# Kernel tuning notes

Measured on AMD Instinct MI355X. Metric: run time of the kernel, lower is better.

## Reference

```python
import jax, jax.numpy as jnp
import numpy as np

# Analytic closed form of the 4-qubit circuit. Wires (0,1) and (2,3) are
# independent 2-qubit blocks: RY(x_a)oRY(x_b) -> CNOT(a,b) -> RY(p_a)oRY(p_b).
# Heisenberg picture gives:
#   <Z_a> = cos(p_a)*cos(x_a) + sin(p_a)*sin(x_a)*sin(x_b)
#   <Z_b> = cos(p_b)*cos(x_a)*cos(x_b) + sin(p_b)*sin(x_b)

def setup_inputs() -> dict:
    key = jax.random.key(0)
    k1, k2, k3, k4 = jax.random.split(key, 4)
    B = 16384
    return {
        "x": jax.random.uniform(k1, (B, 1, 28, 28), dtype=jnp.float32),
        "vqc_params": jax.random.normal(k2, (4,), dtype=jnp.float32),
        "fc_w": jax.random.normal(k3, (10, 784), dtype=jnp.float32) * 0.05,
        "fc_b": jax.random.normal(k4, (10,), dtype=jnp.float32) * 0.05,
        "bias": jnp.zeros((10,), dtype=jnp.float32),
    }


def _pair_expvals(xa, xb, pa, pb):
    # xa, xb: [B, 196]; pa, pb: scalars
    za = jnp.cos(pa) * jnp.cos(xa) + jnp.sin(pa) * jnp.sin(xa) * jnp.sin(xb)
    zb = jnp.cos(pb) * jnp.cos(xa) * jnp.cos(xb) + jnp.sin(pb) * jnp.sin(xb)
    return za, zb


def reference(x, vqc_params, fc_w, fc_b, bias):
    B = x.shape[0]
    # Extract 2x2 patches in the same (r, c) row-major order as the torch loop.
    # [B,28,28] -> [B,14,2,14,2] -> [B,14,14,2,2] -> [B,196,4]
    p = x[:, 0].reshape(B, 14, 2, 14, 2).transpose(0, 1, 3, 2, 4).reshape(B, 196, 4)
    x0, x1, x2, x3 = p[..., 0], p[..., 1], p[..., 2], p[..., 3]
    p0, p1, p2, p3 = vqc_params[0], vqc_params[1], vqc_params[2], vqc_params[3]
    z0, z1 = _pair_expvals(x0, x1, p0, p1)
    z2, z3 = _pair_expvals(x2, x3, p2, p3)
    q = jnp.stack([z0, z1, z2, z3], axis=-1).reshape(B, 4 * 196)  # patch-major, wire-minor
    logits = q @ fc_w.T + fc_b - bias
    return jax.nn.log_softmax(logits, axis=-1)
```

## Files before the change

kernel.cpp:

```cpp
#include <hip/hip_runtime.h>


typedef __attribute__((ext_vector_type(8))) short short8;
typedef __attribute__((ext_vector_type(4))) float f32x4;

constexpr int WAVES = 4;
constexpr int BLOCK = WAVES * 64;
constexpr int IMGS  = 16;
constexpr int NITER = 7;
constexpr int PF    = 4;

static __device__ __forceinline__ short f2bf(float f) {
    union { float f; unsigned u; } v; v.f = f;
    unsigned r = v.u + 0x7fffu + ((v.u >> 16) & 1u);
    return (short)(r >> 16);
}

__global__ __launch_bounds__(BLOCK, 4)
void quanv_mfma(const float* __restrict__ x,
                const float* __restrict__ vqc,
                const float* __restrict__ fc_w,
                const float* __restrict__ fc_b,
                const float* __restrict__ bias,
                float* __restrict__ out,
                int B)
{
    __shared__ float cpart[3][64 * 4];

    const int tid  = threadIdx.x;
    const int lane = tid & 63;
    const int wv   = tid >> 6;
    const int i16  = lane & 15;
    const int g    = lane >> 4;

    const int imgBase = blockIdx.x * IMGS;
    const int imgLane = imgBase + i16;
    const long xb = (long)(imgLane < B ? imgLane : B - 1) * 784;
    const float* __restrict__ xpb = x + xb;

    auto xoff = [&](int I) -> int {
        const int kb = wv + 4 * I;
        int j0 = kb * 8 + 2 * g;
        if (j0 > 194) j0 = 0;
        const int r = j0 / 14, c = j0 - 14 * r;
        return 56 * r + 2 * c;
    };

    float4 bT[PF], bB[PF];
    #pragma unroll
    for (int I = 0; I < PF; ++I) {
        const int o = xoff(I);
        bT[I] = *reinterpret_cast<const float4*>(xpb + o);
        bB[I] = *reinterpret_cast<const float4*>(xpb + o + 28);
    }

    float S0, C0, S1, C1, S2, C2, S3, C3;
    __sincosf(vqc[0], &S0, &C0);
    __sincosf(vqc[1], &S1, &C1);
    __sincosf(vqc[2], &S2, &C2);
    __sincosf(vqc[3], &S3, &C3);

    const int ncl = (i16 < 10) ? i16 : 9;
    const float* __restrict__ wrow = fc_w + ncl * 784;
    short8 bf[NITER];
    #pragma unroll
    for (int I = 0; I < NITER; ++I) {
        const int kb = wv + 4 * I;
        int k = kb * 32 + g * 8;
        if (k > 776) k = 776;
        const float4 lo = *reinterpret_cast<const float4*>(wrow + k);
        const float4 hi = *reinterpret_cast<const float4*>(wrow + k + 4);
        short8 t;
        t[0] = f2bf(lo.x); t[1] = f2bf(lo.y); t[2] = f2bf(lo.z); t[3] = f2bf(lo.w);
        t[4] = f2bf(hi.x); t[5] = f2bf(hi.y); t[6] = f2bf(hi.z); t[7] = f2bf(hi.w);
        bf[I] = t;
    }

    f32x4 acc = {0.f, 0.f, 0.f, 0.f};

    #pragma unroll
    for (int I = 0; I < NITER; ++I) {
        const float4 a4 = bT[I & 3];
        const float4 b4 = bB[I & 3];

        if (I + PF < NITER) {
            const int o = xoff(I + PF);
            bT[I & 3] = *reinterpret_cast<const float4*>(xpb + o);
            bB[I & 3] = *reinterpret_cast<const float4*>(xpb + o + 28);
        }

        const int   j0  = (wv + 4 * I) * 8 + 2 * g;
        const float msk = (j0 <= 194) ? 1.f : 0.f;

        float sa, ca, sb, cb, sc, cc, sd, cd;
        __sincosf(a4.x, &sa, &ca);  __sincosf(a4.y, &sb, &cb);
        __sincosf(b4.x, &sc, &cc);  __sincosf(b4.y, &sd, &cd);
        const float q0 = (C0 * ca + S0 * (sa * sb)) * msk;
        const float q1 = (C1 * (ca * cb) + S1 * sb) * msk;
        const float q2 = (C2 * cc + S2 * (sc * sd)) * msk;
        const float q3 = (C3 * (cc * cd) + S3 * sd) * msk;
        __sincosf(a4.z, &sa, &ca);  __sincosf(a4.w, &sb, &cb);
        __sincosf(b4.z, &sc, &cc);  __sincosf(b4.w, &sd, &cd);
        const float q4 = (C0 * ca + S0 * (sa * sb)) * msk;
        const float q5 = (C1 * (ca * cb) + S1 * sb) * msk;
        const float q6 = (C2 * cc + S2 * (sc * sd)) * msk;
        const float q7 = (C3 * (cc * cd) + S3 * sd) * msk;

        short8 a;
        a[0] = f2bf(q0); a[1] = f2bf(q1); a[2] = f2bf(q2); a[3] = f2bf(q3);
        a[4] = f2bf(q4); a[5] = f2bf(q5); a[6] = f2bf(q6); a[7] = f2bf(q7);

        acc = __builtin_amdgcn_mfma_f32_16x16x32_bf16(a, bf[I], acc, 0, 0, 0);
    }

    if (wv > 0)
        *reinterpret_cast<f32x4*>(&cpart[wv - 1][lane * 4]) = acc;
    __syncthreads();

    if (wv == 0) {
        #pragma unroll
        for (int p = 0; p < 3; ++p)
            acc += *reinterpret_cast<const f32x4*>(&cpart[p][lane * 4]);
        const float bk = (i16 < 10) ? (fc_b[i16] - bias[i16]) : 0.f;

        #pragma unroll
        for (int r = 0; r < 4; ++r) {
            const float lg = acc[r] + bk;
            float mx = (i16 < 10) ? lg : -3.0e38f;
            #pragma unroll
            for (int off = 1; off < 16; off <<= 1)
                mx = fmaxf(mx, __shfl_xor(mx, off, 64));
            float s = (i16 < 10) ? __expf(lg - mx) : 0.f;
            #pragma unroll
            for (int off = 1; off < 16; off <<= 1)
                s += __shfl_xor(s, off, 64);
            const int im = imgBase + g * 4 + r;
            if (i16 < 10 && im < B)
                out[(long)im * 10 + i16] = lg - mx - __logf(s);
        }
    }
}

extern "C" void kernel_launch(void* const* d_in, const int* in_sizes, int n_in,
                              void* d_out, int out_size, void* d_ws, size_t ws_size,
                              hipStream_t stream) {
    const float* x    = (const float*)d_in[0];
    const float* vqc  = (const float*)d_in[1];
    const float* fc_w = (const float*)d_in[2];
    const float* fc_b = (const float*)d_in[3];
    const float* bias = (const float*)d_in[4];
    float* outp = (float*)d_out;

    const int B = in_sizes[0] / 784;
    const int nblocks = (B + IMGS - 1) / IMGS;
    hipLaunchKernelGGL(quanv_mfma, dim3(nblocks), dim3(BLOCK), 0, stream,
                       x, vqc, fc_w, fc_b, bias, outp, B);
}
```

Baseline: 17.20 us.

## Stage quantum features through LDS with coalesced float4 loads and packed bf16 conversion

The block now loads its 16 images with fully coalesced float4 reads across all threads, computes the expectation values, and writes packed bf16 features into a shared-memory tile laid out in patch-major order. The MFMA loop then reads A fragments from LDS instead of doing strided per-lane global loads and redundant masked trig on padding. Software bf16 rounding is replaced with the hardware v_cvt_pk_bf16_f32 instruction. This adds about 25 KB of LDS per block and an extra barrier, which may lower occupancy, and it drops the register prefetch pipeline.

```diff
diff --git a/kernel.cpp b/kernel.cpp
--- a/kernel.cpp
+++ b/kernel.cpp
@@ -8,12 +8,12 @@
 constexpr int BLOCK = WAVES * 64;
 constexpr int IMGS  = 16;
 constexpr int NITER = 7;
-constexpr int PF    = 4;
+constexpr int S2    = 800;
 
-static __device__ __forceinline__ short f2bf(float f) {
-    union { float f; unsigned u; } v; v.f = f;
-    unsigned r = v.u + 0x7fffu + ((v.u >> 16) & 1u);
-    return (short)(r >> 16);
+static __device__ __forceinline__ unsigned pkbf2(float lo, float hi) {
+    unsigned r;
+    asm("v_cvt_pk_bf16_f32 %0, %1, %2" : "=v"(r) : "v"(lo), "v"(hi));
+    return r;
 }
 
 __global__ __launch_bounds__(BLOCK, 4)
@@ -25,6 +25,7 @@
                 float* __restrict__ out,
                 int B)
 {
+    __shared__ __align__(16) unsigned short q_lds[IMGS * S2];
     __shared__ float cpart[3][64 * 4];
 
     const int tid  = threadIdx.x;
@@ -32,85 +33,77 @@
     const int wv   = tid >> 6;
     const int i16  = lane & 15;
     const int g    = lane >> 4;
+    const int imgBase = blockIdx.x * IMGS;
 
-    const int imgBase = blockIdx.x * IMGS;
-    const int imgLane = imgBase + i16;
-    const long xb = (long)(imgLane < B ? imgLane : B - 1) * 784;
-    const float* __restrict__ xpb = x + xb;
-
-    auto xoff = [&](int I) -> int {
-        const int kb = wv + 4 * I;
-        int j0 = kb * 8 + 2 * g;
-        if (j0 > 194) j0 = 0;
-        const int r = j0 / 14, c = j0 - 14 * r;
-        return 56 * r + 2 * c;
-    };
-
-    float4 bT[PF], bB[PF];
-    #pragma unroll
-    for (int I = 0; I < PF; ++I) {
-        const int o = xoff(I);
-        bT[I] = *reinterpret_cast<const float4*>(xpb + o);
-        bB[I] = *reinterpret_cast<const float4*>(xpb + o + 28);
-    }
-
-    float S0, C0, S1, C1, S2, C2, S3, C3;
+    float S0, C0, S1, C1, S2p, C2p, S3, C3;
     __sincosf(vqc[0], &S0, &C0);
     __sincosf(vqc[1], &S1, &C1);
-    __sincosf(vqc[2], &S2, &C2);
+    __sincosf(vqc[2], &S2p, &C2p);
     __sincosf(vqc[3], &S3, &C3);
+
+    const float4* __restrict__ xf4 =
+        reinterpret_cast<const float4*>(x) + (long)imgBase * 196;
+    #pragma unroll
+    for (int it = 0; it < 13; ++it) {
+        const unsigned u = it * BLOCK + tid;
+        if (it < 12 || u < 3136u) {
+            const float4 v = xf4[u];
+            const unsigned img = u / 196u;
+            const unsigned jv  = u - 196u * img;
+            const unsigned y   = jv / 7u;
+            const unsigned cx  = jv - 7u * y;
+            const unsigned par = y & 1u;
+
+            const float CA = par ? C2p : C0, SA = par ? S2p : S0;
+            const float CB = par ? C3  : C1, SB = par ? S3  : S1;
+
+            float sa, ca, sb, cb;
+            __sincosf(v.x, &sa, &ca);  __sincosf(v.y, &sb, &cb);
+            const float za1 = CA * ca + SA * (sa * sb);
+            const float zb1 = CB * (ca * cb) + SB * sb;
+            __sincosf(v.z, &sa, &ca);  __sincosf(v.w, &sb, &cb);
+            const float za2 = CA * ca + SA * (sa * sb);
+            const float zb2 = CB * (ca * cb) + SB * sb;
+
+            const unsigned qb = ((y >> 1) * 14u + 2u * cx) * 4u + 2u * par;
+            const unsigned e  = img * S2 + qb;
+            *reinterpret_cast<unsigned*>(&q_lds[e])     = pkbf2(za1, zb1);
+            *reinterpret_cast<unsigned*>(&q_lds[e + 4]) = pkbf2(za2, zb2);
+        }
+    }
+    if (tid < 128) {
+        const int img = tid >> 3, o = (tid & 7) << 1;
+        *reinterpret_cast<unsigned*>(&q_lds[img * S2 + 784 + o]) = 0u;
+    }
 
     const int ncl = (i16 < 10) ? i16 : 9;
     const float* __restrict__ wrow = fc_w + ncl * 784;
     short8 bf[NITER];
     #pragma unroll
     for (int I = 0; I < NITER; ++I) {
-        const int kb = wv + 4 * I;
-        int k = kb * 32 + g * 8;
-        if (k > 776) k = 776;
-        const float4 lo = *reinterpret_cast<const float4*>(wrow + k);
-        const float4 hi = *reinterpret_cast<const float4*>(wrow + k + 4);
-        short8 t;
-        t[0] = f2bf(lo.x); t[1] = f2bf(lo.y); t[2] = f2bf(lo.z); t[3] = f2bf(lo.w);
-        t[4] = f2bf(hi.x); t[5] = f2bf(hi.y); t[6] = f2bf(hi.z); t[7] = f2bf(hi.w);
-        bf[I] = t;
+        int kb = wv + 4 * I; if (kb > 24) kb = 24;
+        int k  = kb * 32 + 8 * g; if (k > 776) k = 776;
+        const float4 lo4 = *reinterpret_cast<const float4*>(wrow + k);
+        const float4 hi4 = *reinterpret_cast<const float4*>(wrow + k + 4);
+        union { unsigned u[4]; short8 s; } t;
+        t.u[0] = pkbf2(lo4.x, lo4.y);
+        t.u[1] = pkbf2(lo4.z, lo4.w);
+        t.u[2] = pkbf2(hi4.x, hi4.y);
+        t.u[3] = pkbf2(hi4.z, hi4.w);
+        bf[I] = t.s;
     }
 
+    __syncthreads();
+
     f32x4 acc = {0.f, 0.f, 0.f, 0.f};
-
     #pragma unroll
     for (int I = 0; I < NITER; ++I) {
-        const float4 a4 = bT[I & 3];
-        const float4 b4 = bB[I & 3];
-
-        if (I + PF < NITER) {
-            const int o = xoff(I + PF);
-            bT[I & 3] = *reinterpret_cast<const float4*>(xpb + o);
-            bB[I & 3] = *reinterpret_cast<const float4*>(xpb + o + 28);
+        const int kb = wv + 4 * I;
+        if (kb < 25) {
+            const short8 a = *reinterpret_cast<const short8*>(
+                &q_lds[i16 * S2 + kb * 32 + 8 * g]);
+            acc = __builtin_amdgcn_mfma_f32_16x16x32_bf16(a, bf[I], acc, 0, 0, 0);
         }
-
-        const int   j0  = (wv + 4 * I) * 8 + 2 * g;
-        const float msk = (j0 <= 194) ? 1.f : 0.f;
-
-        float sa, ca, sb, cb, sc, cc, sd, cd;
-        __sincosf(a4.x, &sa, &ca);  __sincosf(a4.y, &sb, &cb);
-        __sincosf(b4.x, &sc, &cc);  __sincosf(b4.y, &sd, &cd);
-        const float q0 = (C0 * ca + S0 * (sa * sb)) * msk;
-        const float q1 = (C1 * (ca * cb) + S1 * sb) * msk;
-        const float q2 = (C2 * cc + S2 * (sc * sd)) * msk;
-        const float q3 = (C3 * (cc * cd) + S3 * sd) * msk;
-        __sincosf(a4.z, &sa, &ca);  __sincosf(a4.w, &sb, &cb);
-        __sincosf(b4.z, &sc, &cc);  __sincosf(b4.w, &sd, &cd);
-        const float q4 = (C0 * ca + S0 * (sa * sb)) * msk;
-        const float q5 = (C1 * (ca * cb) + S1 * sb) * msk;
-        const float q6 = (C2 * cc + S2 * (sc * sd)) * msk;
-        const float q7 = (C3 * (cc * cd) + S3 * sd) * msk;
-
-        short8 a;
-        a[0] = f2bf(q0); a[1] = f2bf(q1); a[2] = f2bf(q2); a[3] = f2bf(q3);
-        a[4] = f2bf(q4); a[5] = f2bf(q5); a[6] = f2bf(q6); a[7] = f2bf(q7);
-
-        acc = __builtin_amdgcn_mfma_f32_16x16x32_bf16(a, bf[I], acc, 0, 0, 0);
     }
 
     if (wv > 0)
```

Result: slower. 17.99 us (+4.6%).
